# Optimization experiments

Measured on AMD Instinct MI355X. Metric: run time of the kernel, lower is better.

## Reference

```python
import jax, jax.numpy as jnp
import numpy as np

N_QUBITS = 8
N_LAYERS = 4


def _apply_1q(state, U, q):
    """Apply a 2x2 gate U (shape (2,2) shared, or (B,2,2) per-sample) on qubit q.
    state: (B, 2, 2, ..., 2) with qubit q on axis q+1 (wire 0 = most significant)."""
    a = q + 1
    st = jnp.moveaxis(state, a, -1)
    shp = st.shape
    st = st.reshape(shp[0], -1, 2)  # (B, rest, 2)
    if U.ndim == 3:
        st = jnp.einsum('bij,brj->bri', U, st)
    else:
        st = jnp.einsum('ij,brj->bri', U, st)
    return jnp.moveaxis(st.reshape(shp), -1, a)


def _cnot(state, c, t):
    ac, at = c + 1, t + 1
    s0 = jnp.take(state, 0, axis=ac)
    s1 = jnp.take(state, 1, axis=ac)
    at2 = at - 1 if at > ac else at  # axis shift after removing control axis
    s1 = jnp.flip(s1, axis=at2)      # X on target where control = 1
    return jnp.stack([s0, s1], axis=ac)


def _rx(t):
    c = jnp.cos(t / 2)
    s = jnp.sin(t / 2)
    return jnp.stack([jnp.stack([c + 0j, -1j * s]),
                      jnp.stack([-1j * s, c + 0j])]).astype(jnp.complex64)


def _ry(t):
    c = jnp.cos(t / 2)
    s = jnp.sin(t / 2)
    return jnp.stack([jnp.stack([c, -s]),
                      jnp.stack([s, c])]).astype(jnp.complex64)


def _rz(t):
    return jnp.diag(jnp.stack([jnp.exp(-1j * t / 2),
                               jnp.exp(1j * t / 2)])).astype(jnp.complex64)


def _ry_batched(t):
    # t: (B,) -> (B, 2, 2)
    c = jnp.cos(t / 2)
    s = jnp.sin(t / 2)
    U = jnp.stack([jnp.stack([c, -s], axis=-1),
                   jnp.stack([s, c], axis=-1)], axis=-2)
    return U.astype(jnp.complex64)


def setup_inputs() -> dict:
    key = jax.random.key(0)
    k1, k2 = jax.random.split(key)
    B = 16384
    x = jax.random.normal(k1, (B, N_QUBITS), dtype=jnp.float32)
    weights = jax.random.normal(k2, (N_QUBITS * N_LAYERS * 3,), dtype=jnp.float32) * 0.1
    return {"x": x, "weights": weights}


def reference(x, weights):
    n, L = N_QUBITS, N_LAYERS
    B = x.shape[0]
    state = jnp.zeros((B,) + (2,) * n, dtype=jnp.complex64)
    state = state.at[(slice(None),) + (0,) * n].set(1.0)

    # angle encoding: per-sample RY on each wire
    for q in range(n):
        state = _apply_1q(state, _ry_batched(x[:, q]), q)

    idx = 0
    for _ in range(L):
        for q in range(n):
            state = _apply_1q(state, _rx(weights[idx]), q)
            state = _apply_1q(state, _ry(weights[idx + 1]), q)
            state = _apply_1q(state, _rz(weights[idx + 2]), q)
            idx += 3
        for q in range(n - 1):
            state = _cnot(state, q, q + 1)

    p = jnp.abs(state) ** 2  # (B, 2, ..., 2) float32
    outs = []
    for q in range(n):
        axes = tuple(a for a in range(1, n + 1) if a != q + 1)
        z = p.sum(axis=axes)  # (B, 2)
        outs.append(z[:, 0] - z[:, 1])
    return jnp.stack(outs, axis=-1).astype(jnp.float32)
```

## Files before the change

### kernel.cpp

```cpp
#include <hip/hip_runtime.h>


#define NGATES 32

typedef float v2f __attribute__((ext_vector_type(2)));

__device__ __forceinline__ v2f mk2(float a, float b) { v2f t; t.x = a; t.y = b; return t; }

constexpr bool selon(int l, int d) {
    return (l == 0) ? (d == 0) : (((d + l - 1) & (l - 1)) == (l - 1));
}
constexpr int lm_of(int l, int q) {
    int m = 0;
    for (int d = 0; q + d <= 7; ++d)
        if ((l & d) == d) { int qq = q + d; if (qq <= 3) m |= 1 << (3 - qq); }
    return m;
}
constexpr int rm_of(int l, int q) {
    int m = 0;
    for (int d = 0; q + d <= 7; ++d)
        if ((l & d) == d) { int qq = q + d; if (qq >= 4) m |= 1 << (7 - qq); }
    return m;
}
constexpr int slm_of(int l, int q) {
    int m = 0;
    for (int d = 0; d <= q; ++d)
        if (selon(l, d)) { int k = q - d; if (k <= 3) m |= 1 << (3 - k); }
    return m;
}
constexpr int srm_of(int l, int q) {
    int m = 0;
    for (int d = 0; d <= q; ++d)
        if (selon(l, d)) { int k = q - d; if (k >= 4) m |= 1 << (7 - k); }
    return m;
}

__device__ __forceinline__ float xsgn(float f, unsigned m) {
    return __int_as_float(__float_as_int(f) ^ (int)m);
}


template<int C>
__device__ __forceinline__ int dppmov(int x) {
    return __builtin_amdgcn_update_dpp(x, x, C, 0xF, 0xF, false);
}
template<int M>
__device__ __forceinline__ float shx_dpp(float v) {
    int x = __float_as_int(v);
    if constexpr (M == 1)       { x = dppmov<0xB1>(x); }
    else if constexpr (M == 2)  { x = dppmov<0x4E>(x); }
    else if constexpr (M == 3)  { x = dppmov<0x1B>(x); }
    else if constexpr (M == 7)  { x = dppmov<0x141>(x); }
    else if constexpr (M == 8)  { x = dppmov<0x128>(x); }
    else                        { x = dppmov<0x140>(x); }
    return __int_as_float(x);
}
template<int M>
__device__ __forceinline__ float shx_ds(float v) {
    return __int_as_float(__builtin_amdgcn_ds_swizzle(__float_as_int(v), (M << 10) | 0x1F));
}
constexpr bool sgl(int M) {
    return M == 1 || M == 2 || M == 3 || M == 7 || M == 8 || M == 15;
}
template<int M>
__device__ __forceinline__ float shxm(float v) {
    if constexpr (sgl(M)) return shx_dpp<M>(v);
    else                  return shx_ds<M>(v);
}

__device__ __forceinline__ v2f cplx4(v2f K0, v2f K1, v2f A, v2f B) {
    v2f n;
    asm("v_pk_mul_f32 %0, %1, %2 op_sel:[0,0] op_sel_hi:[0,1]"
        : "=v"(n) : "v"(K0), "v"(A));
    asm("v_pk_fma_f32 %0, %1, %2, %0 op_sel:[1,1,0] op_sel_hi:[1,0,1] neg_lo:[1,0,0]"
        : "+v"(n) : "v"(K0), "v"(A));
    asm("v_pk_fma_f32 %0, %1, %2, %0 op_sel:[0,0,0] op_sel_hi:[0,1,1]"
        : "+v"(n) : "v"(K1), "v"(B));
    asm("v_pk_fma_f32 %0, %1, %2, %0 op_sel:[1,1,0] op_sel_hi:[1,0,1] neg_lo:[1,0,0]"
        : "+v"(n) : "v"(K1), "v"(B));
    return n;
}

template<int LM, int RM, int SLM, int SRM>
__device__ __forceinline__ void apply_gate(v2f A[16], int lane, const float4 g)
{
    unsigned sm = 0;
    if constexpr (SLM != 0)
        sm = (unsigned)((__builtin_popcount(lane & SLM) & 1) << 31);
    v2f K0[2], K1[2];
    K0[0] = mk2(g.x, xsgn(g.y, sm));
    K0[1] = mk2(g.x, xsgn(g.y, sm ^ 0x80000000u));
    K1[0] = mk2(xsgn(g.z, sm), g.w);
    K1[1] = mk2(xsgn(g.z, sm ^ 0x80000000u), g.w);

    if constexpr (RM == 0) {
        #pragma unroll
        for (int r = 0; r < 16; ++r) {
            const int v = __builtin_popcount(r & SRM) & 1;
            v2f B = mk2(shxm<LM>(A[r].x), shxm<LM>(A[r].y));
            A[r] = cplx4(K0[v], K1[v], A[r], B);
        }
    } else {
        #pragma unroll
        for (int r = 0; r < 16; ++r) {
            const int p = r ^ RM;
            if (p < r) continue;
            v2f Br, Bp;
            if constexpr (LM != 0) {
                Br = mk2(shxm<LM>(A[p].x), shxm<LM>(A[p].y));
                Bp = mk2(shxm<LM>(A[r].x), shxm<LM>(A[r].y));
            } else {
                Br = A[p];
                Bp = A[r];
            }
            const int vr = __builtin_popcount(r & SRM) & 1;
            const int vp = __builtin_popcount(p & SRM) & 1;
            v2f nr = cplx4(K0[vr], K1[vr], A[r], Br);
            v2f np = cplx4(K0[vp], K1[vp], A[p], Bp);
            A[r] = nr; A[p] = np;
        }
    }
}

#define GATE(L, Q) apply_gate<lm_of(L,Q), rm_of(L,Q), slm_of(L,Q), srm_of(L,Q)>( \
                       A, lane, gsh4[(L)*8+(Q)])
#define LAYER(L) GATE(L,0); GATE(L,1); GATE(L,2); GATE(L,3); \
                 GATE(L,4); GATE(L,5); GATE(L,6); GATE(L,7);

__global__ __launch_bounds__(256, 4) void qsim(const float* __restrict__ x,
                                               const float* __restrict__ w,
                                               float* __restrict__ out, int B)
{
    __shared__ float4 gsh4[NGATES];

    const int tid = threadIdx.x;
    if (tid < NGATES) {
        float hx = 0.5f * w[tid*3+0];
        float hy = 0.5f * w[tid*3+1];
        float hz = 0.5f * w[tid*3+2];
        float cx = cosf(hx), sx = sinf(hx);
        float cy = cosf(hy), sy = sinf(hy);
        float cz = cosf(hz), sz = sinf(hz);
        float m00r = cy*cx,  m00i =  sy*sx;
        float m01r = -sy*cx, m01i = -cy*sx;
        gsh4[tid] = make_float4(cz*m00r + sz*m00i,
                                cz*m00i - sz*m00r,
                                cz*m01r + sz*m01i,
                                cz*m01i - sz*m01r);
    }
    __syncthreads();

    const int lane = tid & 63;
    const int il   = lane & 15;
    const int sample = blockIdx.x * 16 + (tid >> 4);
    if (sample >= B) return;

    const float4* xp = (const float4*)(x + sample * 8);
    float4 xa = xp[0], xb = xp[1];
    float xs[8] = {xa.x, xa.y, xa.z, xa.w, xb.x, xb.y, xb.z, xb.w};
    float cq[8], sq[8];
    #pragma unroll
    for (int q = 0; q < 8; ++q) {
        float h = 0.5f * xs[q];
        __sincosf(h, &sq[q], &cq[q]);
    }
    float lp = ((il & 8) ? sq[0] : cq[0]);
    lp      *= ((il & 4) ? sq[1] : cq[1]);
    lp      *= ((il & 2) ? sq[2] : cq[2]);
    lp      *= ((il & 1) ? sq[3] : cq[3]);
    float t67[4] = {cq[6]*cq[7], cq[6]*sq[7], sq[6]*cq[7], sq[6]*sq[7]};
    float a5[2]  = {cq[5], sq[5]};
    float a4[2]  = {cq[4]*lp, sq[4]*lp};
    v2f A[16];
    #pragma unroll
    for (int r = 0; r < 16; ++r)
        A[r] = mk2(a4[(r >> 3) & 1] * a5[(r >> 2) & 1] * t67[r & 3], 0.f);

    LAYER(0)
    LAYER(1)
    LAYER(2)
    LAYER(3)

    float p[16];
    #pragma unroll
    for (int r = 0; r < 16; ++r) p[r] = A[r].x*A[r].x + A[r].y*A[r].y;

    float s0[8], d0[8];
    #pragma unroll
    for (int k = 0; k < 8; ++k) { s0[k] = p[2*k] + p[2*k+1]; d0[k] = p[2*k] - p[2*k+1]; }
    float A0 = ((d0[0]+d0[1]) + (d0[2]+d0[3])) + ((d0[4]+d0[5]) + (d0[6]+d0[7]));
    float s1[4], d1[4];
    #pragma unroll
    for (int k = 0; k < 4; ++k) { s1[k] = s0[2*k] + s0[2*k+1]; d1[k] = s0[2*k] - s0[2*k+1]; }
    float A1 = (d1[0]+d1[1]) + (d1[2]+d1[3]);
    float s2[2], d2[2];
    #pragma unroll
    for (int k = 0; k < 2; ++k) { s2[k] = s1[2*k] + s1[2*k+1]; d2[k] = s1[2*k] - s1[2*k+1]; }
    float A2 = d2[0] + d2[1];
    float A3 = s2[0] - s2[1];
    float P  = s2[0] + s2[1];

    const unsigned sg1 = (unsigned)(il & 1) << 31;
    const unsigned sg2 = (unsigned)(il & 2) << 30;
    const unsigned sg4 = (unsigned)(il & 4) << 29;
    const unsigned sg8 = (unsigned)(il & 8) << 28;

    float wP = P;
    { float t = shxm<1>(wP); wP = t + xsgn(wP, sg1); }
    { float t = shxm<2>(wP); wP = t + xsgn(wP, sg2); }
    { float t = shxm<4>(wP); wP = t + xsgn(wP, sg4); }
    { float t = shxm<8>(wP); wP = t + xsgn(wP, sg8); }

    float a3 = xsgn(A3, sg8);
    a3 += shxm<1>(a3); a3 += shxm<2>(a3); a3 += shxm<4>(a3); a3 += shxm<8>(a3);
    float a2 = xsgn(A2, sg4);
    a2 += shxm<1>(a2); a2 += shxm<2>(a2); a2 += shxm<4>(a2); a2 += shxm<8>(a2);
    float a1 = xsgn(A1, sg2);
    a1 += shxm<1>(a1); a1 += shxm<2>(a1); a1 += shxm<4>(a1); a1 += shxm<8>(a1);
    float a0 = xsgn(A0, sg1);
    a0 += shxm<1>(a0); a0 += shxm<2>(a0); a0 += shxm<4>(a0); a0 += shxm<8>(a0);

    float* op = out + sample * 8;
    if (il == 8)      { op[0] = wP; op[4] = a3; }
    else if (il == 4) { op[1] = wP; op[5] = a2; }
    else if (il == 2) { op[2] = wP; op[6] = a1; }
    else if (il == 1) { op[3] = wP; op[7] = a0; }
}

extern "C" void kernel_launch(void* const* d_in, const int* in_sizes, int n_in,
                              void* d_out, int out_size, void* d_ws, size_t ws_size,
                              hipStream_t stream) {
    const float* x = (const float*)d_in[0];
    const float* w = (const float*)d_in[1];
    float* out = (float*)d_out;
    const int B = in_sizes[0] / 8;
    const int blocks = (B + 15) / 16;
    qsim<<<blocks, 256, 0, stream>>>(x, w, out, B);
}
```

Before: 78.66 us.

## Split each sample's state across 32 lanes with 8 amplitudes per lane

Changes the state layout from 16 lanes holding 16 complex amplitudes each to 32 lanes holding 8 each, so five qubits live across lanes and three in registers. Cross-lane permutations for masks 4-6 and 9-14 are now built from two chained DPP moves instead of ds_swizzle, and launch bounds are raised to 8 waves per SIMD to use the lower register footprint. The aim is more parallelism and occupancy per sample. The cost is more cross-lane shuffles per gate, with some masks needing two DPP hops, and an extra reduction stage at the end.

Result: slower. 82.80 us (+5.3%).

```diff
diff --git a/kernel.cpp b/kernel.cpp
--- a/kernel.cpp
+++ b/kernel.cpp
@@ -10,35 +10,26 @@
 constexpr bool selon(int l, int d) {
     return (l == 0) ? (d == 0) : (((d + l - 1) & (l - 1)) == (l - 1));
 }
-constexpr int lm_of(int l, int q) {
+constexpr int fpm(int l, int q) {
     int m = 0;
     for (int d = 0; q + d <= 7; ++d)
-        if ((l & d) == d) { int qq = q + d; if (qq <= 3) m |= 1 << (3 - qq); }
+        if ((l & d) == d) m |= 1 << (7 - (q + d));
     return m;
 }
-constexpr int rm_of(int l, int q) {
-    int m = 0;
-    for (int d = 0; q + d <= 7; ++d)
-        if ((l & d) == d) { int qq = q + d; if (qq >= 4) m |= 1 << (7 - qq); }
-    return m;
-}
-constexpr int slm_of(int l, int q) {
+constexpr int fsm(int l, int q) {
     int m = 0;
     for (int d = 0; d <= q; ++d)
-        if (selon(l, d)) { int k = q - d; if (k <= 3) m |= 1 << (3 - k); }
+        if (selon(l, d)) m |= 1 << (7 - (q - d));
     return m;
 }
-constexpr int srm_of(int l, int q) {
-    int m = 0;
-    for (int d = 0; d <= q; ++d)
-        if (selon(l, d)) { int k = q - d; if (k >= 4) m |= 1 << (7 - k); }
-    return m;
-}
+constexpr int lm_of (int l, int q) { return fpm(l, q) >> 3; }
+constexpr int rm_of (int l, int q) { return fpm(l, q) & 7;  }
+constexpr int slm_of(int l, int q) { return fsm(l, q) >> 3; }
+constexpr int srm_of(int l, int q) { return fsm(l, q) & 7;  }
 
 __device__ __forceinline__ float xsgn(float f, unsigned m) {
     return __int_as_float(__float_as_int(f) ^ (int)m);
 }
-
 
 template<int C>
 __device__ __forceinline__ int dppmov(int x) {
@@ -50,8 +41,17 @@
     if constexpr (M == 1)       { x = dppmov<0xB1>(x); }
     else if constexpr (M == 2)  { x = dppmov<0x4E>(x); }
     else if constexpr (M == 3)  { x = dppmov<0x1B>(x); }
+    else if constexpr (M == 4)  { x = dppmov<0x1B>(x);  x = dppmov<0x141>(x); }
+    else if constexpr (M == 5)  { x = dppmov<0x4E>(x);  x = dppmov<0x141>(x); }
+    else if constexpr (M == 6)  { x = dppmov<0xB1>(x);  x = dppmov<0x141>(x); }
     else if constexpr (M == 7)  { x = dppmov<0x141>(x); }
     else if constexpr (M == 8)  { x = dppmov<0x128>(x); }
+    else if constexpr (M == 9)  { x = dppmov<0xB1>(x);  x = dppmov<0x128>(x); }
+    else if constexpr (M == 10) { x = dppmov<0x4E>(x);  x = dppmov<0x128>(x); }
+    else if constexpr (M == 11) { x = dppmov<0x1B>(x);  x = dppmov<0x128>(x); }
+    else if constexpr (M == 12) { x = dppmov<0x140>(x); x = dppmov<0x1B>(x);  }
+    else if constexpr (M == 13) { x = dppmov<0x140>(x); x = dppmov<0x4E>(x);  }
+    else if constexpr (M == 14) { x = dppmov<0x140>(x); x = dppmov<0xB1>(x);  }
     else                        { x = dppmov<0x140>(x); }
     return __int_as_float(x);
 }
@@ -59,12 +59,9 @@
 __device__ __forceinline__ float shx_ds(float v) {
     return __int_as_float(__builtin_amdgcn_ds_swizzle(__float_as_int(v), (M << 10) | 0x1F));
 }
-constexpr bool sgl(int M) {
-    return M == 1 || M == 2 || M == 3 || M == 7 || M == 8 || M == 15;
-}
 template<int M>
 __device__ __forceinline__ float shxm(float v) {
-    if constexpr (sgl(M)) return shx_dpp<M>(v);
+    if constexpr (M < 16) return shx_dpp<M>(v);
     else                  return shx_ds<M>(v);
 }
 
@@ -82,7 +79,7 @@
 }
 
 template<int LM, int RM, int SLM, int SRM>
-__device__ __forceinline__ void apply_gate(v2f A[16], int lane, const float4 g)
+__device__ __forceinline__ void apply_gate(v2f A[8], int lane, const float4 g)
 {
     unsigned sm = 0;
     if constexpr (SLM != 0)
@@ -95,14 +92,14 @@
 
     if constexpr (RM == 0) {
         #pragma unroll
-        for (int r = 0; r < 16; ++r) {
+        for (int r = 0; r < 8; ++r) {
             const int v = __builtin_popcount(r & SRM) & 1;
             v2f B = mk2(shxm<LM>(A[r].x), shxm<LM>(A[r].y));
             A[r] = cplx4(K0[v], K1[v], A[r], B);
         }
     } else {
         #pragma unroll
-        for (int r = 0; r < 16; ++r) {
+        for (int r = 0; r < 8; ++r) {
             const int p = r ^ RM;
             if (p < r) continue;
             v2f Br, Bp;
@@ -127,7 +124,7 @@
 #define LAYER(L) GATE(L,0); GATE(L,1); GATE(L,2); GATE(L,3); \
                  GATE(L,4); GATE(L,5); GATE(L,6); GATE(L,7);
 
-__global__ __launch_bounds__(256, 4) void qsim(const float* __restrict__ x,
+__global__ __launch_bounds__(256, 8) void qsim(const float* __restrict__ x,
                                                const float* __restrict__ w,
                                                float* __restrict__ out, int B)
 {
@@ -151,8 +148,8 @@
     __syncthreads();
 
     const int lane = tid & 63;
-    const int il   = lane & 15;
-    const int sample = blockIdx.x * 16 + (tid >> 4);
+    const int il   = lane & 31;
+    const int sample = blockIdx.x * 8 + (tid >> 5);
     if (sample >= B) return;
 
     const float4* xp = (const float4*)(x + sample * 8);
@@ -164,67 +161,65 @@
         float h = 0.5f * xs[q];
         __sincosf(h, &sq[q], &cq[q]);
     }
-    float lp = ((il & 8) ? sq[0] : cq[0]);
-    lp      *= ((il & 4) ? sq[1] : cq[1]);
-    lp      *= ((il & 2) ? sq[2] : cq[2]);
-    lp      *= ((il & 1) ? sq[3] : cq[3]);
+    float lp = ((il & 16) ? sq[0] : cq[0]);
+    lp      *= ((il &  8) ? sq[1] : cq[1]);
+    lp      *= ((il &  4) ? sq[2] : cq[2]);
+    lp      *= ((il &  2) ? sq[3] : cq[3]);
+    lp      *= ((il &  1) ? sq[4] : cq[4]);
     float t67[4] = {cq[6]*cq[7], cq[6]*sq[7], sq[6]*cq[7], sq[6]*sq[7]};
-    float a5[2]  = {cq[5], sq[5]};
-    float a4[2]  = {cq[4]*lp, sq[4]*lp};
-    v2f A[16];
-    #pragma unroll
-    for (int r = 0; r < 16; ++r)
-        A[r] = mk2(a4[(r >> 3) & 1] * a5[(r >> 2) & 1] * t67[r & 3], 0.f);
+    float a5[2]  = {cq[5]*lp, sq[5]*lp};
+    v2f A[8];
+    #pragma unroll
+    for (int r = 0; r < 8; ++r)
+        A[r] = mk2(a5[(r >> 2) & 1] * t67[r & 3], 0.f);
 
     LAYER(0)
     LAYER(1)
     LAYER(2)
     LAYER(3)
 
-    float p[16];
-    #pragma unroll
-    for (int r = 0; r < 16; ++r) p[r] = A[r].x*A[r].x + A[r].y*A[r].y;
-
-    float s0[8], d0[8];
-    #pragma unroll
-    for (int k = 0; k < 8; ++k) { s0[k] = p[2*k] + p[2*k+1]; d0[k] = p[2*k] - p[2*k+1]; }
-    float A0 = ((d0[0]+d0[1]) + (d0[2]+d0[3])) + ((d0[4]+d0[5]) + (d0[6]+d0[7]));
-    float s1[4], d1[4];
-    #pragma unroll
-    for (int k = 0; k < 4; ++k) { s1[k] = s0[2*k] + s0[2*k+1]; d1[k] = s0[2*k] - s0[2*k+1]; }
-    float A1 = (d1[0]+d1[1]) + (d1[2]+d1[3]);
-    float s2[2], d2[2];
-    #pragma unroll
-    for (int k = 0; k < 2; ++k) { s2[k] = s1[2*k] + s1[2*k+1]; d2[k] = s1[2*k] - s1[2*k+1]; }
-    float A2 = d2[0] + d2[1];
-    float A3 = s2[0] - s2[1];
-    float P  = s2[0] + s2[1];
-
-    const unsigned sg1 = (unsigned)(il & 1) << 31;
-    const unsigned sg2 = (unsigned)(il & 2) << 30;
-    const unsigned sg4 = (unsigned)(il & 4) << 29;
-    const unsigned sg8 = (unsigned)(il & 8) << 28;
+    float p[8];
+    #pragma unroll
+    for (int r = 0; r < 8; ++r) p[r] = A[r].x*A[r].x + A[r].y*A[r].y;
+
+    float s0[4], d0[4];
+    #pragma unroll
+    for (int k = 0; k < 4; ++k) { s0[k] = p[2*k] + p[2*k+1]; d0[k] = p[2*k] - p[2*k+1]; }
+    float Ab0 = (d0[0]+d0[1]) + (d0[2]+d0[3]);
+    float s1a = s0[0] + s0[1], s1b = s0[2] + s0[3];
+    float Ab1 = (s0[0]-s0[1]) + (s0[2]-s0[3]);
+    float Ab2 = s1a - s1b;
+    float P   = s1a + s1b;
+
+    const unsigned sg1  = (unsigned)(il & 1)  << 31;
+    const unsigned sg2  = (unsigned)(il & 2)  << 30;
+    const unsigned sg4  = (unsigned)(il & 4)  << 29;
+    const unsigned sg8  = (unsigned)(il & 8)  << 28;
+    const unsigned sg16 = (unsigned)(il & 16) << 27;
 
     float wP = P;
-    { float t = shxm<1>(wP); wP = t + xsgn(wP, sg1); }
-    { float t = shxm<2>(wP); wP = t + xsgn(wP, sg2); }
-    { float t = shxm<4>(wP); wP = t + xsgn(wP, sg4); }
-    { float t = shxm<8>(wP); wP = t + xsgn(wP, sg8); }
-
-    float a3 = xsgn(A3, sg8);
-    a3 += shxm<1>(a3); a3 += shxm<2>(a3); a3 += shxm<4>(a3); a3 += shxm<8>(a3);
-    float a2 = xsgn(A2, sg4);
-    a2 += shxm<1>(a2); a2 += shxm<2>(a2); a2 += shxm<4>(a2); a2 += shxm<8>(a2);
-    float a1 = xsgn(A1, sg2);
-    a1 += shxm<1>(a1); a1 += shxm<2>(a1); a1 += shxm<4>(a1); a1 += shxm<8>(a1);
-    float a0 = xsgn(A0, sg1);
-    a0 += shxm<1>(a0); a0 += shxm<2>(a0); a0 += shxm<4>(a0); a0 += shxm<8>(a0);
+    { float t = shxm<1>(wP);  wP = t + xsgn(wP, sg1);  }
+    { float t = shxm<2>(wP);  wP = t + xsgn(wP, sg2);  }
+    { float t = shxm<4>(wP);  wP = t + xsgn(wP, sg4);  }
+    { float t = shxm<8>(wP);  wP = t + xsgn(wP, sg8);  }
+    { float t = shxm<16>(wP); wP = t + xsgn(wP, sg16); }
+
+    float a5v = xsgn(Ab2, sg8);
+    a5v += shxm<1>(a5v); a5v += shxm<2>(a5v); a5v += shxm<4>(a5v);
+    a5v += shxm<8>(a5v); a5v += shxm<16>(a5v);
+    float a6v = xsgn(Ab1, sg4);
+    a6v += shxm<1>(a6v); a6v += shxm<2>(a6v); a6v += shxm<4>(a6v);
+    a6v += shxm<8>(a6v); a6v += shxm<16>(a6v);
+    float a7v = xsgn(Ab0, sg2);
+    a7v += shxm<1>(a7v); a7v += shxm<2>(a7v); a7v += shxm<4>(a7v);
+    a7v += shxm<8>(a7v); a7v += shxm<16>(a7v);
 
     float* op = out + sample * 8;
-    if (il == 8)      { op[0] = wP; op[4] = a3; }
-    else if (il == 4) { op[1] = wP; op[5] = a2; }
-    else if (il == 2) { op[2] = wP; op[6] = a1; }
-    else if (il == 1) { op[3] = wP; op[7] = a0; }
+    if (il == 16)      { op[0] = wP; op[5] = a5v; }
+    else if (il == 8)  { op[1] = wP; op[6] = a6v; }
+    else if (il == 4)  { op[2] = wP; op[7] = a7v; }
+    else if (il == 2)  { op[3] = wP; }
+    else if (il == 17) { op[4] = wP; }
 }
 
 extern "C" void kernel_launch(void* const* d_in, const int* in_sizes, int n_in,
@@ -234,6 +229,6 @@
     const float* w = (const float*)d_in[1];
     float* out = (float*)d_out;
     const int B = in_sizes[0] / 8;
-    const int blocks = (B + 15) / 16;
+    const int blocks = (B + 7) / 8;
     qsim<<<blocks, 256, 0, stream>>>(x, w, out, B);
 }
```
